# Kernel optimization log

Measured on AMD Instinct MI355X. Metric: run time of the kernel, lower is better.

The kernel has to match this reference:

```python
import jax, jax.numpy as jnp
import numpy as np

# ---- BD layout (byte-decoded token format) ----
MARK_AX = 0; OP_MUL = 1
ALU_LO = 16; ALU_HI = 32
AX_CARRY_LO = 48; AX_CARRY_HI = 64
OUTPUT_LO = 80; OUTPUT_HI = 96
BD_DIM = 128
# ---- GenericE layout ----
N_POS = 8; GE_DIM = 64
NIB_A = 0; NIB_B = 1; OP_START = 2; RESULT = 40
OPCODE = 27
HID = 256


def setup_inputs() -> dict:
    key = jax.random.key(0)
    k1, k2, k3 = jax.random.split(key, 3)
    x_bd = jax.random.uniform(k1, (8, 8192, BD_DIM), dtype=jnp.float32)
    W1 = jax.random.normal(k2, (GE_DIM, HID), dtype=jnp.float32) * 0.05
    b1 = jnp.zeros((HID,), dtype=jnp.float32)
    W2 = jax.random.normal(k3, (HID, GE_DIM), dtype=jnp.float32) * 0.05
    b2 = jnp.zeros((GE_DIM,), dtype=jnp.float32)
    return {"x_bd": x_bd, "W1": W1, "b1": b1, "W2": W2, "b2": b2}


def reference(x_bd, W1, b1, W2, b2):
    B, S, _ = x_bd.shape
    # active-token mask: skip unless MARK_AX >= 0.5 AND OP_MUL >= 0.5
    mask = (x_bd[..., MARK_AX] >= 0.5) & (x_bd[..., OP_MUL] >= 0.5)  # [B,S]

    # bd_to_ge: decode nibble one-hots into byte operands (per token, vectorized)
    a_lo = jnp.argmax(x_bd[..., ALU_LO:ALU_LO + 16], axis=-1)
    a_hi = jnp.argmax(x_bd[..., ALU_HI:ALU_HI + 16], axis=-1)
    byte_a = (a_lo + (a_hi << 4)).astype(x_bd.dtype)                 # [B,S]
    b_lo = jnp.argmax(x_bd[..., AX_CARRY_LO:AX_CARRY_LO + 16], axis=-1)
    b_hi = jnp.argmax(x_bd[..., AX_CARRY_HI:AX_CARRY_HI + 16], axis=-1)
    byte_b = (b_lo + (b_hi << 4)).astype(x_bd.dtype)                 # [B,S]

    # build GE tensor [B,S,N_POS,GE_DIM]
    x_ge = jnp.zeros((B, S, N_POS, GE_DIM), dtype=x_bd.dtype)
    x_ge = x_ge.at[..., 0, NIB_A].set(byte_a)
    x_ge = x_ge.at[..., 0, NIB_B].set(byte_b)
    x_ge = x_ge.at[..., :, OP_START + OPCODE].set(1.0)

    # tiny MLP (mul_layers) applied to every position of every token
    h = jax.nn.relu(x_ge @ W1 + b1)        # [B,S,N_POS,HID]
    y = h @ W2 + b2                        # [B,S,N_POS,GE_DIM]

    # ge_to_bd: decode RESULT byte, split into nibbles, scatter +2.0 one-hots
    res = jnp.round(y[..., 0, RESULT]).astype(jnp.int32) & 255       # [B,S]
    r_lo = res & 15
    r_hi = (res >> 4) & 15

    m = mask.astype(x_bd.dtype)[..., None]                           # [B,S,1]
    out = x_bd.at[..., OUTPUT_LO:OUTPUT_LO + 16].add(
        2.0 * m * jax.nn.one_hot(r_lo, 16, dtype=x_bd.dtype))
    out = out.at[..., OUTPUT_HI:OUTPUT_HI + 16].add(
        2.0 * m * jax.nn.one_hot(r_hi, 16, dtype=x_bd.dtype))
    return out
```

## Files before the change

### kernel.cpp

```cpp
#include <hip/hip_runtime.h>
#include <math.h>


#define HID 256

__global__ __launch_bounds__(256) void ebm_fused_kernel(
    const float* __restrict__ x,
    const float* __restrict__ W1,
    const float* __restrict__ b1,
    const float* __restrict__ W2,
    const float* __restrict__ b2,
    float* __restrict__ out,
    int tokens)
{
    const int tid = threadIdx.x;
    const int c = tid & 31;

    float r0[8], r1[8], r29[8], rb1[8], w2c[8];
    #pragma unroll
    for (int k = 0; k < 8; ++k) {
        const int j = c + 32 * k;
        r0[k]  = W1[j];
        r1[k]  = W1[HID + j];
        r29[k] = W1[29 * HID + j];
        rb1[k] = b1[j];
        w2c[k] = W2[j * 64 + 40];
    }
    const float b2v = b2[40];

    const int nHW = (gridDim.x * blockDim.x) >> 5;
    const int hw0 = (blockIdx.x * blockDim.x + tid) >> 5;

    const float4* __restrict__ in4  = (const float4*)x;
    float4*       __restrict__ out4 = (float4*)out;

    for (int tok = hw0; tok < tokens; tok += nHW) {
        float4 v = in4[tok * 32 + c];

        int valid = (v.x >= 0.5f) && (v.y >= 0.5f);
        const int mval = __shfl(valid, 0, 32);

        const int fi = (c & 3) << 2;
        float m = v.x; int g = fi;
        if (v.y > m) { m = v.y; g = fi + 1; }
        if (v.z > m) { m = v.z; g = fi + 2; }
        if (v.w > m) { m = v.w; g = fi + 3; }
        {
            float om = __shfl_xor(m, 1, 32);
            int   og = __shfl_xor(g, 1, 32);
            if (om > m || (om == m && og < g)) { m = om; g = og; }
            om = __shfl_xor(m, 2, 32);
            og = __shfl_xor(g, 2, 32);
            if (om > m || (om == m && og < g)) { m = om; g = og; }
        }
        const int a_lo = __shfl(g, 4, 32);
        const int a_hi = __shfl(g, 8, 32);
        const int b_lo = __shfl(g, 12, 32);
        const int b_hi = __shfl(g, 16, 32);

        int res = 0;
        if (__ballot(mval)) {
            const float af = (float)(a_lo | (a_hi << 4));
            const float bf = (float)(b_lo | (b_hi << 4));
            double acc = 0.0;
            #pragma unroll
            for (int k = 0; k < 8; ++k) {
                float t = af * r0[k];
                t += bf * r1[k];
                t += r29[k];
                t += rb1[k];
                t = fmaxf(t, 0.0f);
                acc = fma((double)t, (double)w2c[k], acc);
            }
            acc += __shfl_xor(acc, 16, 32);
            acc += __shfl_xor(acc,  8, 32);
            acc += __shfl_xor(acc,  4, 32);
            acc += __shfl_xor(acc,  2, 32);
            acc += __shfl_xor(acc,  1, 32);
            const double y = acc + (double)b2v;
            res = ((int)rint(y)) & 255;
        }

        const int t_lo = 80 + (res & 15);
        const int t_hi = 96 + ((res >> 4) & 15);
        const float addv = mval ? 2.0f : 0.0f;
        const int e0 = c << 2;
        v.x += (e0     == t_lo || e0     == t_hi) ? addv : 0.0f;
        v.y += (e0 + 1 == t_lo || e0 + 1 == t_hi) ? addv : 0.0f;
        v.z += (e0 + 2 == t_lo || e0 + 2 == t_hi) ? addv : 0.0f;
        v.w += (e0 + 3 == t_lo || e0 + 3 == t_hi) ? addv : 0.0f;

        out4[tok * 32 + c] = v;
    }
}

extern "C" void kernel_launch(void* const* d_in, const int* in_sizes, int n_in,
                              void* d_out, int out_size, void* d_ws, size_t ws_size,
                              hipStream_t stream) {
    const float* x  = (const float*)d_in[0];
    const float* W1 = (const float*)d_in[1];
    const float* b1 = (const float*)d_in[2];
    const float* W2 = (const float*)d_in[3];
    const float* b2 = (const float*)d_in[4];
    float* out = (float*)d_out;

    const int tokens = in_sizes[0] / 128;

    const int block = 256;
    const int grid  = 2048;
    ebm_fused_kernel<<<grid, block, 0, stream>>>(x, W1, b1, W2, b2, out, tokens);
}
```

Baseline: 99.31 us.

## Use one half-wave per token, hoist input load, ballot-based argmax

Drops the grid-stride loop in favour of one 32-lane group per token, launching enough blocks to cover all tokens. The input float4 load is issued before the weight preloads so it is in flight while those run. The argmax tie-break moves from paired value/index shuffles to a max-only shuffle reduction plus a ballot and count-trailing-zeros to pick the first winning lane. In exchange, every block reloads the W1/W2 weight columns, and the grid becomes much larger.

```diff
diff --git a/kernel.cpp b/kernel.cpp
--- a/kernel.cpp
+++ b/kernel.cpp
@@ -3,6 +3,8 @@
 
 
 #define HID 256
+
+typedef float f4 __attribute__((ext_vector_type(4)));
 
 __global__ __launch_bounds__(256) void ebm_fused_kernel(
     const float* __restrict__ x,
@@ -13,8 +15,16 @@
     float* __restrict__ out,
     int tokens)
 {
-    const int tid = threadIdx.x;
-    const int c = tid & 31;
+    const int tid  = threadIdx.x;
+    const int c    = tid & 31;
+    const int tok  = (blockIdx.x * blockDim.x + tid) >> 5;
+    if (tok >= tokens) return;
+
+    const f4* __restrict__ in4  = (const f4*)x;
+    f4*       __restrict__ out4 = (f4*)out;
+
+    const int idx = tok * 32 + c;
+    f4 v = in4[idx];
 
     float r0[8], r1[8], r29[8], rb1[8], w2c[8];
     #pragma unroll
@@ -28,70 +38,63 @@
     }
     const float b2v = b2[40];
 
-    const int nHW = (gridDim.x * blockDim.x) >> 5;
-    const int hw0 = (blockIdx.x * blockDim.x + tid) >> 5;
+    int valid = (v.x >= 0.5f) && (v.y >= 0.5f);
+    const int mval = __shfl(valid, 0, 32);
 
-    const float4* __restrict__ in4  = (const float4*)x;
-    float4*       __restrict__ out4 = (float4*)out;
+    const int fi = (c & 3) << 2;
+    float m = v.x; int g = fi;
+    if (v.y > m) { m = v.y; g = fi + 1; }
+    if (v.z > m) { m = v.z; g = fi + 2; }
+    if (v.w > m) { m = v.w; g = fi + 3; }
 
-    for (int tok = hw0; tok < tokens; tok += nHW) {
-        float4 v = in4[tok * 32 + c];
+    float mm = m;
+    mm = fmaxf(mm, __shfl_xor(mm, 1, 32));
+    mm = fmaxf(mm, __shfl_xor(mm, 2, 32));
 
-        int valid = (v.x >= 0.5f) && (v.y >= 0.5f);
-        const int mval = __shfl(valid, 0, 32);
+    const unsigned long long bal = __ballot(m == mm);
+    const int hwb = tid & 32;
+    const int w0 = 4  + __builtin_ctz((unsigned)(bal >> (hwb + 4))  & 0xFu);
+    const int w1 = 8  + __builtin_ctz((unsigned)(bal >> (hwb + 8))  & 0xFu);
+    const int w2 = 12 + __builtin_ctz((unsigned)(bal >> (hwb + 12)) & 0xFu);
+    const int w3 = 16 + __builtin_ctz((unsigned)(bal >> (hwb + 16)) & 0xFu);
+    const int a_lo = __shfl(g, w0, 32);
+    const int a_hi = __shfl(g, w1, 32);
+    const int b_lo = __shfl(g, w2, 32);
+    const int b_hi = __shfl(g, w3, 32);
 
-        const int fi = (c & 3) << 2;
-        float m = v.x; int g = fi;
-        if (v.y > m) { m = v.y; g = fi + 1; }
-        if (v.z > m) { m = v.z; g = fi + 2; }
-        if (v.w > m) { m = v.w; g = fi + 3; }
-        {
-            float om = __shfl_xor(m, 1, 32);
-            int   og = __shfl_xor(g, 1, 32);
-            if (om > m || (om == m && og < g)) { m = om; g = og; }
-            om = __shfl_xor(m, 2, 32);
-            og = __shfl_xor(g, 2, 32);
-            if (om > m || (om == m && og < g)) { m = om; g = og; }
+    int res = 0;
+    if (__ballot(mval)) {
+        const float af = (float)(a_lo | (a_hi << 4));
+        const float bf = (float)(b_lo | (b_hi << 4));
+        double acc = 0.0;
+        #pragma unroll
+        for (int k = 0; k < 8; ++k) {
+            float t = af * r0[k];
+            t += bf * r1[k];
+            t += r29[k];
+            t += rb1[k];
+            t = fmaxf(t, 0.0f);
+            acc = fma((double)t, (double)w2c[k], acc);
         }
-        const int a_lo = __shfl(g, 4, 32);
-        const int a_hi = __shfl(g, 8, 32);
-        const int b_lo = __shfl(g, 12, 32);
-        const int b_hi = __shfl(g, 16, 32);
+        acc += __shfl_xor(acc, 16, 32);
+        acc += __shfl_xor(acc,  8, 32);
+        acc += __shfl_xor(acc,  4, 32);
+        acc += __shfl_xor(acc,  2, 32);
+        acc += __shfl_xor(acc,  1, 32);
+        const double y = acc + (double)b2v;
+        res = ((int)rint(y)) & 255;
+    }
 
-        int res = 0;
-        if (__ballot(mval)) {
-            const float af = (float)(a_lo | (a_hi << 4));
-            const float bf = (float)(b_lo | (b_hi << 4));
-            double acc = 0.0;
-            #pragma unroll
-            for (int k = 0; k < 8; ++k) {
-                float t = af * r0[k];
-                t += bf * r1[k];
-                t += r29[k];
-                t += rb1[k];
-                t = fmaxf(t, 0.0f);
-                acc = fma((double)t, (double)w2c[k], acc);
-            }
-            acc += __shfl_xor(acc, 16, 32);
-            acc += __shfl_xor(acc,  8, 32);
-            acc += __shfl_xor(acc,  4, 32);
-            acc += __shfl_xor(acc,  2, 32);
-            acc += __shfl_xor(acc,  1, 32);
-            const double y = acc + (double)b2v;
-            res = ((int)rint(y)) & 255;
-        }
+    const int t_lo = 80 + (res & 15);
+    const int t_hi = 96 + ((res >> 4) & 15);
+    const float addv = mval ? 2.0f : 0.0f;
+    const int e0 = c << 2;
+    v.x += (e0     == t_lo || e0     == t_hi) ? addv : 0.0f;
+    v.y += (e0 + 1 == t_lo || e0 + 1 == t_hi) ? addv : 0.0f;
+    v.z += (e0 + 2 == t_lo || e0 + 2 == t_hi) ? addv : 0.0f;
+    v.w += (e0 + 3 == t_lo || e0 + 3 == t_hi) ? addv : 0.0f;
 
-        const int t_lo = 80 + (res & 15);
-        const int t_hi = 96 + ((res >> 4) & 15);
-        const float addv = mval ? 2.0f : 0.0f;
-        const int e0 = c << 2;
-        v.x += (e0     == t_lo || e0     == t_hi) ? addv : 0.0f;
-        v.y += (e0 + 1 == t_lo || e0 + 1 == t_hi) ? addv : 0.0f;
-        v.z += (e0 + 2 == t_lo || e0 + 2 == t_hi) ? addv : 0.0f;
-        v.w += (e0 + 3 == t_lo || e0 + 3 == t_hi) ? addv : 0.0f;
-
-        out4[tok * 32 + c] = v;
-    }
+    out4[idx] = v;
 }
 
 extern "C" void kernel_launch(void* const* d_in, const int* in_sizes, int n_in,
@@ -107,6 +110,6 @@
     const int tokens = in_sizes[0] / 128;
 
     const int block = 256;
-    const int grid  = 2048;
+    const int grid  = (tokens * 32 + block - 1) / block;
     ebm_fused_kernel<<<grid, block, 0, stream>>>(x, W1, b1, W2, b2, out, tokens);
 }
```

After: 102.7 us. 1.03x slower.
